# Kernel optimization log

Measured on AMD Instinct MI355X. Metric: run time of the kernel, lower is better.

The kernel has to match this reference:

```python
import jax, jax.numpy as jnp
import numpy as np

D_MODEL = 1024
N_TILES = 16
BATCH = 32768
THRESH = 0.3


def setup_inputs() -> dict:
    key = jax.random.key(0)
    k_x, k_sig, k_w, k_b = jax.random.split(key, 4)
    x = jax.random.normal(k_x, (BATCH, D_MODEL), dtype=jnp.float32)
    # nn.Parameter(torch.randn(n_tiles, d_model) * 0.5)
    signatures_raw = jax.random.normal(k_sig, (N_TILES, D_MODEL), dtype=jnp.float32) * 0.5
    # nn.Linear(d_model, d_model) default init: U(-1/sqrt(fan_in), 1/sqrt(fan_in))
    bound = 1.0 / np.sqrt(D_MODEL)
    W = jax.random.uniform(k_w, (N_TILES, D_MODEL, D_MODEL), dtype=jnp.float32, minval=-bound, maxval=bound)
    b = jax.random.uniform(k_b, (N_TILES, D_MODEL), dtype=jnp.float32, minval=-bound, maxval=bound)
    return {"x": x, "signatures_raw": signatures_raw, "W": W, "b": b}


def _quantize_ternary(s):
    # straight-through ternary: forward value is q, gradient is identity
    q = jnp.where(s > THRESH, 1.0, jnp.where(s < -THRESH, -1.0, 0.0))
    return s + jax.lax.stop_gradient(q - s)


def reference(x, signatures_raw, W, b):
    sigs = _quantize_ternary(signatures_raw)          # [E, D]
    scores = x @ sigs.T                               # [B, E]
    tile_indices = jnp.argmax(scores, axis=-1)        # [B]
    out = jnp.zeros_like(x)
    # fixed small loop over experts: masked combine of per-expert Linear+ReLU
    for e in range(N_TILES):
        y = jax.nn.relu(x @ W[e].T + b[e])            # [B, D]
        out = out + jnp.where((tile_indices == e)[:, None], y, 0.0)
    out = out + x                                     # residual
    return out, tile_indices
```

## Files before the change

kernel.cpp:

```cpp
#include <hip/hip_runtime.h>
#include <hip/hip_bf16.h>

#define BATCH   32768
#define DM      1024
#define NE      16
#define THRESHF 0.3f
#define MARGIN  0.02f

#define CTRL_OFF 131072
#define QBF_OFF  139264
#define PERM_OFF 172032
#define XBF_OFF  311296
#define WB_OFF   67420160ull
#define WS_NEED  (WB_OFF + (size_t)NE * DM * DM * 2)

typedef __attribute__((ext_vector_type(8))) short bf16x8;
typedef __attribute__((ext_vector_type(4))) float f32x4;

static __device__ __forceinline__ unsigned short f2bf(float f) {
    union { float f; unsigned u; } v; v.f = f;
    unsigned r = (v.u + 0x7FFFu + ((v.u >> 16) & 1u)) >> 16;
    return (unsigned short)r;
}
static __device__ __forceinline__ float bf2f(unsigned short h) {
    union { unsigned u; float f; } v; v.u = ((unsigned)h) << 16;
    return v.f;
}

static __device__ __forceinline__ void gload_lds16(const void* g, void* s) {
    __builtin_amdgcn_global_load_lds(
        (const __attribute__((address_space(1))) void*)g,
        (__attribute__((address_space(3))) void*)s, 16, 0, 0);
}

__global__ void k_init(const float* __restrict__ sig, unsigned* __restrict__ ctrl,
                       int* __restrict__ perm, unsigned short* __restrict__ Qbf) {
    const int t = blockIdx.x * 256 + threadIdx.x;
    if (t < 544) ctrl[t] = 0;
    if (t < 1024) {
        unsigned pm = 0, mm = 0;
#pragma unroll
        for (int e = 0; e < NE; ++e) {
            float s = sig[e * DM + t];
            pm |= (s > THRESHF ? 1u : 0u) << e;
            mm |= (s < -THRESHF ? 1u : 0u) << e;
        }
        ctrl[1024 + t] = pm | (mm << 16);
    }
    if (t < 8704) ((int4*)perm)[t] = make_int4(0, 0, 0, 0);
    {
        float s = sig[t];
        Qbf[t] = s > THRESHF ? (unsigned short)0x3F80u
                             : (s < -THRESHF ? (unsigned short)0xBF80u : (unsigned short)0u);
    }
}

__global__ __launch_bounds__(256) void k_router(const float* __restrict__ x,
                                                const unsigned short* __restrict__ Qbf,
                                                unsigned* __restrict__ ctrl,
                                                int* __restrict__ idx,
                                                float* __restrict__ outIdx,
                                                unsigned short* __restrict__ Xbf,
                                                int writeXbf) {
    const int t = threadIdx.x, w = t >> 6, l = t & 63;
    const int lc = l & 15, lr = l >> 4;
    const int wid = blockIdx.x * 4 + w;
    const int row0 = wid * 16;
    const unsigned* packT = ctrl + 1024;

    const float* ax = x + (size_t)(row0 + lc) * DM + lr * 8;
    const unsigned short* qx = Qbf + (size_t)lc * DM + lr * 8;
    unsigned short* xb = Xbf + (size_t)(row0 + lc) * DM + lr * 8;

    f32x4 acc = (f32x4){0.f, 0.f, 0.f, 0.f};

    for (int kt = 0; kt < 16; ++kt) {
#pragma unroll
        for (int h = 0; h < 2; ++h) {
            const int ko = kt * 64 + h * 32;
            float4 v0 = *(const float4*)(ax + ko);
            float4 v1 = *(const float4*)(ax + ko + 4);
            bf16x8 q = *(const bf16x8*)(qx + ko);

            float f[8] = {v0.x, v0.y, v0.z, v0.w, v1.x, v1.y, v1.z, v1.w};
            bf16x8 ah, al;
#pragma unroll
            for (int j = 0; j < 8; ++j) {
                unsigned short hi = f2bf(f[j]);
                float r = f[j] - bf2f(hi);
                ah[j] = (short)hi;
                al[j] = (short)f2bf(r);
            }
            if (writeXbf) *(bf16x8*)(xb + ko) = ah;
            acc = __builtin_amdgcn_mfma_f32_16x16x32_bf16(ah, q, acc, 0, 0, 0);
            acc = __builtin_amdgcn_mfma_f32_16x16x32_bf16(al, q, acc, 0, 0, 0);
        }
    }

    float bv[4]; int bi[4]; float gap[4];
#pragma unroll
    for (int reg = 0; reg < 4; ++reg) {
        float v = acc[reg]; int i = lc; float s = -3.4e38f;
#pragma unroll
        for (int m = 1; m < 16; m <<= 1) {
            float ov = __shfl_xor(v, m, 64);
            int oi = __shfl_xor(i, m, 64);
            float os = __shfl_xor(s, m, 64);
            bool take = (ov > v) || (ov == v && oi < i);
            float loser = take ? v : ov;
            v = take ? ov : v;
            i = take ? oi : i;
            s = fmaxf(fmaxf(s, os), loser);
        }
        bv[reg] = v; bi[reg] = i; gap[reg] = v - s;
    }

    unsigned flagsw = 0;
#pragma unroll
    for (int reg = 0; reg < 4; ++reg)
        flagsw |= (gap[reg] < MARGIN ? 1u : 0u) << reg;

    if (__any(lc == 0 && flagsw != 0)) {
#pragma unroll
        for (int reg = 0; reg < 4; ++reg) {
            for (int g = 0; g < 4; ++g) {
                const unsigned fw = __shfl(flagsw, g * 16, 64);
                if ((fw >> reg) & 1u) {
                    const int row = row0 + g * 4 + reg;
                    const float* xr = x + (size_t)row * DM;
                    float xv[16]; unsigned mk[16];
#pragma unroll
                    for (int k2 = 0; k2 < 16; ++k2) {
                        xv[k2] = xr[k2 * 64 + l];
                        mk[k2] = packT[k2 * 64 + l];
                    }
                    double best = 0.0; int bbi = 0;
                    for (int e = 0; e < 16; ++e) {
                        double a = 0.0;
#pragma unroll
                        for (int k2 = 0; k2 < 16; ++k2) {
                            const int pb = (int)((mk[k2] >> e) & 1u);
                            const int mb = (int)((mk[k2] >> (16 + e)) & 1u);
                            a += pb ? (double)xv[k2] : (mb ? -(double)xv[k2] : 0.0);
                        }
#pragma unroll
                        for (int m = 1; m < 64; m <<= 1) a += __shfl_xor(a, m, 64);
                        if (e == 0 || a > best) { best = a; bbi = e; }
                    }
                    if (lr == g && lc == 0) bi[reg] = bbi;
                }
            }
        }
    }

    if (lc == 0) {
#pragma unroll
        for (int reg = 0; reg < 4; ++reg) {
            const int row = row0 + lr * 4 + reg;
            idx[row] = bi[reg];
            outIdx[row] = (float)bi[reg];
            atomicAdd(&ctrl[bi[reg] * 16], 1u);
        }
    }
}

__global__ void k_scan(unsigned* __restrict__ ctrl) {
    if (threadIdx.x == 0) {
        int* tileBase = (int*)(ctrl + 512);
        int acc = 0;
        for (int e = 0; e < NE; ++e) {
            tileBase[e] = acc;
            acc += (int)((ctrl[e * 16] + 127u) / 128u);
        }
        tileBase[NE] = acc;
    }
}

__global__ __launch_bounds__(256) void k_perm(const int* __restrict__ idx,
                                              unsigned* __restrict__ ctrl,
                                              int* __restrict__ perm) {
    __shared__ unsigned hcnt[16];
    __shared__ unsigned hbase[16];
    const int t = threadIdx.x;
    const int row = blockIdx.x * 256 + t;
    const int* tileBase = (const int*)(ctrl + 512);
    if (t < 16) hcnt[t] = 0;
    __syncthreads();
    const int e = idx[row];
    const unsigned lrank = atomicAdd(&hcnt[e], 1u);
    __syncthreads();
    if (t < 16) hbase[t] = atomicAdd(&ctrl[256 + t * 16], hcnt[t]);
    __syncthreads();
    perm[tileBase[e] * 128 + hbase[e] + lrank] = row;
}

__global__ __launch_bounds__(256) void k_convw(const float* __restrict__ W,
                                               unsigned short* __restrict__ Wb) {
    const size_t g = ((size_t)blockIdx.x * 256 + threadIdx.x) * 8;
    float4 a = *(const float4*)&W[g];
    float4 b = *(const float4*)&W[g + 4];
    *(ushort4*)&Wb[g]     = make_ushort4(f2bf(a.x), f2bf(a.y), f2bf(a.z), f2bf(a.w));
    *(ushort4*)&Wb[g + 4] = make_ushort4(f2bf(b.x), f2bf(b.y), f2bf(b.z), f2bf(b.w));
}

template <int MODE>
__global__ __launch_bounds__(256) void k_gemm(const unsigned short* __restrict__ Xbf,
                                              const unsigned short* __restrict__ Wb,
                                              const float* __restrict__ x,
                                              const float* __restrict__ W,
                                              const float* __restrict__ bias,
                                              const int* __restrict__ perm,
                                              const unsigned* __restrict__ ctrl,
                                              float* __restrict__ out) {
    __shared__ unsigned short A_lds[2][128 * 32];
    __shared__ unsigned short B_lds[2][128 * 32];

    const int* tileBase = (const int*)(ctrl + 512);

    int bx, ny;
    {
        const int flat = blockIdx.x;
        const int xcd = flat & 7, s2 = flat >> 3;
        bx = xcd * 34 + (s2 >> 3);
        ny = s2 & 7;
    }
    const int total = tileBase[NE];
    if (bx >= total) return;
    int e = 0;
    while (e < NE - 1 && tileBase[e + 1] <= bx) ++e;
    const int ltile = bx - tileBase[e];
    const int valid = (int)ctrl[e * 16] - ltile * 128;
    const int n0 = ny * 128;

    const int t = threadIdx.x, w = t >> 6, l = t & 63;
    const int wr = w >> 1, wc = w & 1;
    const int lc = l & 15, lr = l >> 4;
    const int hsw = ((t & 3) - ((t >> 3) & 3)) & 3;
    const int ssw = (lr + (lc >> 1)) & 3;

    f32x4 acc[4][4];
#pragma unroll
    for (int m = 0; m < 4; ++m)
#pragma unroll
        for (int n = 0; n < 4; ++n) acc[m][n] = (f32x4){0.f, 0.f, 0.f, 0.f};

    const size_t aRowBase = (size_t)bx * 128;
    const unsigned short* Bg = Wb + ((size_t)e * DM + n0) * DM;

    if (MODE == 0) {
        const int r0 = t >> 2;
        const int prow0 = perm[aRowBase + r0];
        const int prow1 = perm[aRowBase + 64 + r0];
        const unsigned short* a0 = Xbf + (size_t)prow0 * DM + hsw * 8;
        const unsigned short* a1 = Xbf + (size_t)prow1 * DM + hsw * 8;

        gload_lds16(a0, &A_lds[0][(size_t)(w * 64) * 8]);
        gload_lds16(a1, &A_lds[0][(size_t)(256 + w * 64) * 8]);
#pragma unroll
        for (int rd = 0; rd < 2; ++rd) {
            const int c = rd * 256 + t;
            gload_lds16(Bg + (size_t)(c >> 2) * DM + hsw * 8,
                        &B_lds[0][(size_t)(rd * 256 + w * 64) * 8]);
        }
        __syncthreads();

        int cur = 0;
        for (int kt = 0; kt < DM / 32; ++kt) {
            if (kt < DM / 32 - 1) {
                const int ko = (kt + 1) * 32;
                gload_lds16(a0 + ko, &A_lds[cur ^ 1][(size_t)(w * 64) * 8]);
                gload_lds16(a1 + ko, &A_lds[cur ^ 1][(size_t)(256 + w * 64) * 8]);
#pragma unroll
                for (int rd = 0; rd < 2; ++rd) {
                    const int c = rd * 256 + t;
                    gload_lds16(Bg + (size_t)(c >> 2) * DM + ko + hsw * 8,
                                &B_lds[cur ^ 1][(size_t)(rd * 256 + w * 64) * 8]);
                }
            }

            bf16x8 af[4], bf[4];
#pragma unroll
            for (int m = 0; m < 4; ++m)
                af[m] = *(const bf16x8*)&A_lds[cur][(wr * 64 + m * 16 + lc) * 32 + ssw * 8];
#pragma unroll
            for (int n = 0; n < 4; ++n)
                bf[n] = *(const bf16x8*)&B_lds[cur][(wc * 64 + n * 16 + lc) * 32 + ssw * 8];
#pragma unroll
            for (int m = 0; m < 4; ++m)
#pragma unroll
                for (int n = 0; n < 4; ++n)
                    acc[m][n] = __builtin_amdgcn_mfma_f32_16x16x32_bf16(af[m], bf[n], acc[m][n], 0, 0, 0);

            if (kt < DM / 32 - 1) __syncthreads();
            cur ^= 1;
        }
    } else {
        for (int kt = 0; kt < DM / 32; ++kt) {
            __syncthreads();
#pragma unroll
            for (int rd = 0; rd < 2; ++rd) {
                const int c = rd * 256 + t;
                const int r = c >> 2;
                const float* wp = W + ((size_t)e * DM + n0 + r) * DM + kt * 32 + hsw * 8;
                float4 b0 = *(const float4*)wp;
                float4 b1 = *(const float4*)(wp + 4);
                *(ushort4*)&B_lds[0][c * 8]     = make_ushort4(f2bf(b0.x), f2bf(b0.y), f2bf(b0.z), f2bf(b0.w));
                *(ushort4*)&B_lds[0][c * 8 + 4] = make_ushort4(f2bf(b1.x), f2bf(b1.y), f2bf(b1.z), f2bf(b1.w));
                ushort4 p0 = make_ushort4(0, 0, 0, 0), p1 = p0;
                if (r < valid) {
                    const int orow = perm[aRowBase + r];
                    const float* xp = x + (size_t)orow * DM + kt * 32 + hsw * 8;
                    float4 q0 = *(const float4*)xp;
                    float4 q1 = *(const float4*)(xp + 4);
                    p0 = make_ushort4(f2bf(q0.x), f2bf(q0.y), f2bf(q0.z), f2bf(q0.w));
                    p1 = make_ushort4(f2bf(q1.x), f2bf(q1.y), f2bf(q1.z), f2bf(q1.w));
                }
                *(ushort4*)&A_lds[0][c * 8]     = p0;
                *(ushort4*)&A_lds[0][c * 8 + 4] = p1;
            }
            __syncthreads();

            bf16x8 af[4], bf[4];
#pragma unroll
            for (int m = 0; m < 4; ++m)
                af[m] = *(const bf16x8*)&A_lds[0][(wr * 64 + m * 16 + lc) * 32 + ssw * 8];
#pragma unroll
            for (int n = 0; n < 4; ++n)
                bf[n] = *(const bf16x8*)&B_lds[0][(wc * 64 + n * 16 + lc) * 32 + ssw * 8];
#pragma unroll
            for (int m = 0; m < 4; ++m)
#pragma unroll
                for (int n = 0; n < 4; ++n)
                    acc[m][n] = __builtin_amdgcn_mfma_f32_16x16x32_bf16(af[m], bf[n], acc[m][n], 0, 0, 0);
        }
    }

    float bv[4];
#pragma unroll
    for (int n = 0; n < 4; ++n) bv[n] = bias[e * DM + n0 + wc * 64 + n * 16 + lc];

#pragma unroll
    for (int m = 0; m < 4; ++m) {
#pragma unroll
        for (int reg = 0; reg < 4; ++reg) {
            const int rit = wr * 64 + m * 16 + lr * 4 + reg;
            if (rit < valid) {
                const int orow = perm[aRowBase + rit];
                float* op = out + (size_t)orow * DM;
                if (MODE == 0) {
                    const unsigned short* xr = Xbf + (size_t)orow * DM;
#pragma unroll
                    for (int n = 0; n < 4; ++n) {
                        const int col = n0 + wc * 64 + n * 16 + lc;
                        float v = acc[m][n][reg] + bv[n];
                        v = v > 0.f ? v : 0.f;
                        op[col] = v + bf2f(xr[col]);
                    }
                } else {
                    const float* xr = x + (size_t)orow * DM;
#pragma unroll
                    for (int n = 0; n < 4; ++n) {
                        const int col = n0 + wc * 64 + n * 16 + lc;
                        float v = acc[m][n][reg] + bv[n];
                        v = v > 0.f ? v : 0.f;
                        op[col] = v + xr[col];
                    }
                }
            }
        }
    }
}

extern "C" void kernel_launch(void* const* d_in, const int* in_sizes, int n_in,
                              void* d_out, int out_size, void* d_ws, size_t ws_size,
                              hipStream_t stream) {
    const float* x    = (const float*)d_in[0];
    const float* sig  = (const float*)d_in[1];
    const float* W    = (const float*)d_in[2];
    const float* bias = (const float*)d_in[3];
    float* out = (float*)d_out;
    float* outIdx = out + (size_t)BATCH * DM;

    char* ws = (char*)d_ws;
    int* idx = (int*)ws;
    unsigned* ctrl = (unsigned*)(ws + CTRL_OFF);
    unsigned short* Qbf = (unsigned short*)(ws + QBF_OFF);
    int* perm = (int*)(ws + PERM_OFF);
    unsigned short* Xbf = (unsigned short*)(ws + XBF_OFF);
    unsigned short* Wb = (unsigned short*)(ws + WB_OFF);

    const bool full = ws_size >= WS_NEED;

    k_init<<<64, 256, 0, stream>>>(sig, ctrl, perm, Qbf);
    k_router<<<512, 256, 0, stream>>>(x, Qbf, ctrl, idx, outIdx, Xbf, full ? 1 : 0);
    k_scan<<<1, 64, 0, stream>>>(ctrl);
    k_perm<<<128, 256, 0, stream>>>(idx, ctrl, perm);
    if (full) {
        k_convw<<<8192, 256, 0, stream>>>(W, Wb);
        k_gemm<0><<<2176, 256, 0, stream>>>(Xbf, Wb, x, W, bias, perm, ctrl, out);
    } else {
        k_gemm<1><<<2176, 256, 0, stream>>>(Xbf, Wb, x, W, bias, perm, ctrl, out);
    }
}
```

Measured before the change: 251.4 us.

## Use triple-buffered LDS pipeline with a single barrier per k-step in bf16 GEMM

The bf16 GEMM main loop moves from double buffering to a three-stage LDS ring, issuing global-to-LDS loads two k-steps ahead. An explicit vmcnt wait plus one s_barrier per iteration replaces the trailing __syncthreads, so loads get more time to land while MFMAs run. In exchange LDS use grows from 32KB to 48KB per block, which may cut occupancy. The vmcnt(4) count relies on each stage issuing exactly four loads.

```diff
diff --git a/kernel.cpp b/kernel.cpp
--- a/kernel.cpp
+++ b/kernel.cpp
@@ -212,8 +212,8 @@
                                               const int* __restrict__ perm,
                                               const unsigned* __restrict__ ctrl,
                                               float* __restrict__ out) {
-    __shared__ unsigned short A_lds[2][128 * 32];
-    __shared__ unsigned short B_lds[2][128 * 32];
+    __shared__ unsigned short A_lds[3][128 * 32];
+    __shared__ unsigned short B_lds[3][128 * 32];
 
     const int* tileBase = (const int*)(ctrl + 512);
 
@@ -253,29 +253,32 @@
         const int prow1 = perm[aRowBase + 64 + r0];
         const unsigned short* a0 = Xbf + (size_t)prow0 * DM + hsw * 8;
         const unsigned short* a1 = Xbf + (size_t)prow1 * DM + hsw * 8;
-
-        gload_lds16(a0, &A_lds[0][(size_t)(w * 64) * 8]);
-        gload_lds16(a1, &A_lds[0][(size_t)(256 + w * 64) * 8]);
-#pragma unroll
-        for (int rd = 0; rd < 2; ++rd) {
-            const int c = rd * 256 + t;
-            gload_lds16(Bg + (size_t)(c >> 2) * DM + hsw * 8,
-                        &B_lds[0][(size_t)(rd * 256 + w * 64) * 8]);
-        }
-        __syncthreads();
-
+        const unsigned short* b0 = Bg + (size_t)(t >> 2) * DM + hsw * 8;
+        const unsigned short* b1 = Bg + (size_t)(64 + (t >> 2)) * DM + hsw * 8;
+
+        auto STAGE = [&](int kt, int buf) {
+            const int ko = kt * 32;
+            gload_lds16(a0 + ko, &A_lds[buf][(size_t)(w * 64) * 8]);
+            gload_lds16(a1 + ko, &A_lds[buf][(size_t)(256 + w * 64) * 8]);
+            gload_lds16(b0 + ko, &B_lds[buf][(size_t)(w * 64) * 8]);
+            gload_lds16(b1 + ko, &B_lds[buf][(size_t)(256 + w * 64) * 8]);
+        };
+
+        STAGE(0, 0);
+        STAGE(1, 1);
+
+        const int NT = DM / 32;
         int cur = 0;
-        for (int kt = 0; kt < DM / 32; ++kt) {
-            if (kt < DM / 32 - 1) {
-                const int ko = (kt + 1) * 32;
-                gload_lds16(a0 + ko, &A_lds[cur ^ 1][(size_t)(w * 64) * 8]);
-                gload_lds16(a1 + ko, &A_lds[cur ^ 1][(size_t)(256 + w * 64) * 8]);
-#pragma unroll
-                for (int rd = 0; rd < 2; ++rd) {
-                    const int c = rd * 256 + t;
-                    gload_lds16(Bg + (size_t)(c >> 2) * DM + ko + hsw * 8,
-                                &B_lds[cur ^ 1][(size_t)(rd * 256 + w * 64) * 8]);
-                }
+        for (int kt = 0; kt < NT; ++kt) {
+            if (kt + 1 < NT) asm volatile("s_waitcnt vmcnt(4)" ::: "memory");
+            else             asm volatile("s_waitcnt vmcnt(0)" ::: "memory");
+            __builtin_amdgcn_sched_barrier(0);
+            __builtin_amdgcn_s_barrier();
+            __builtin_amdgcn_sched_barrier(0);
+
+            if (kt + 2 < NT) {
+                const int nb = (cur + 2 >= 3) ? cur - 1 : cur + 2;
+                STAGE(kt + 2, nb);
             }
 
             bf16x8 af[4], bf[4];
@@ -291,8 +294,7 @@
                 for (int n = 0; n < 4; ++n)
                     acc[m][n] = __builtin_amdgcn_mfma_f32_16x16x32_bf16(af[m], bf[n], acc[m][n], 0, 0, 0);
 
-            if (kt < DM / 32 - 1) __syncthreads();
-            cur ^= 1;
+            cur = (cur + 1 >= 3) ? 0 : cur + 1;
         }
     } else {
         for (int kt = 0; kt < DM / 32; ++kt) {
@@ -302,18 +304,18 @@
                 const int c = rd * 256 + t;
                 const int r = c >> 2;
                 const float* wp = W + ((size_t)e * DM + n0 + r) * DM + kt * 32 + hsw * 8;
-                float4 b0 = *(const float4*)wp;
-                float4 b1 = *(const float4*)(wp + 4);
-                *(ushort4*)&B_lds[0][c * 8]     = make_ushort4(f2bf(b0.x), f2bf(b0.y), f2bf(b0.z), f2bf(b0.w));
-                *(ushort4*)&B_lds[0][c * 8 + 4] = make_ushort4(f2bf(b1.x), f2bf(b1.y), f2bf(b1.z), f2bf(b1.w));
+                float4 q0 = *(const float4*)wp;
+                float4 q1 = *(const float4*)(wp + 4);
+                *(ushort4*)&B_lds[0][c * 8]     = make_ushort4(f2bf(q0.x), f2bf(q0.y), f2bf(q0.z), f2bf(q0.w));
+                *(ushort4*)&B_lds[0][c * 8 + 4] = make_ushort4(f2bf(q1.x), f2bf(q1.y), f2bf(q1.z), f2bf(q1.w));
                 ushort4 p0 = make_ushort4(0, 0, 0, 0), p1 = p0;
                 if (r < valid) {
                     const int orow = perm[aRowBase + r];
                     const float* xp = x + (size_t)orow * DM + kt * 32 + hsw * 8;
-                    float4 q0 = *(const float4*)xp;
-                    float4 q1 = *(const float4*)(xp + 4);
-                    p0 = make_ushort4(f2bf(q0.x), f2bf(q0.y), f2bf(q0.z), f2bf(q0.w));
-                    p1 = make_ushort4(f2bf(q1.x), f2bf(q1.y), f2bf(q1.z), f2bf(q1.w));
+                    float4 u0 = *(const float4*)xp;
+                    float4 u1 = *(const float4*)(xp + 4);
+                    p0 = make_ushort4(f2bf(u0.x), f2bf(u0.y), f2bf(u0.z), f2bf(u0.w));
+                    p1 = make_ushort4(f2bf(u1.x), f2bf(u1.y), f2bf(u1.z), f2bf(u1.w));
                 }
                 *(ushort4*)&A_lds[0][c * 8]     = p0;
                 *(ushort4*)&A_lds[0][c * 8 + 4] = p1;
@@ -335,9 +337,9 @@
         }
     }
 
-    float bv[4];
-#pragma unroll
-    for (int n = 0; n < 4; ++n) bv[n] = bias[e * DM + n0 + wc * 64 + n * 16 + lc];
+    float bvv[4];
+#pragma unroll
+    for (int n = 0; n < 4; ++n) bvv[n] = bias[e * DM + n0 + wc * 64 + n * 16 + lc];
 
 #pragma unroll
     for (int m = 0; m < 4; ++m) {
@@ -352,7 +354,7 @@
 #pragma unroll
                     for (int n = 0; n < 4; ++n) {
                         const int col = n0 + wc * 64 + n * 16 + lc;
-                        float v = acc[m][n][reg] + bv[n];
+                        float v = acc[m][n][reg] + bvv[n];
                         v = v > 0.f ? v : 0.f;
                         op[col] = v + bf2f(xr[col]);
                     }
@@ -361,7 +363,7 @@
 #pragma unroll
                     for (int n = 0; n < 4; ++n) {
                         const int col = n0 + wc * 64 + n * 16 + lc;
-                        float v = acc[m][n][reg] + bv[n];
+                        float v = acc[m][n][reg] + bvv[n];
                         v = v > 0.f ? v : 0.f;
                         op[col] = v + xr[col];
                     }
```

Measured after the change: 247.8 us. About the same (-1.4%).
